# Kernel tuning notes

Measured on AMD Instinct MI355X. Metric: run time of the kernel, lower is better.

The kernel has to match this reference:

```python
import jax, jax.numpy as jnp
import numpy as np

N_NODES = 100000
N_EDGES = 3200000
D_FEAT = 16


def scatter_mean(src, index, num_segments):
    # src: [E, d], index: [E] -> [num_segments, d]; mean over incident edges,
    # with count clamped to 1 (matches torch_scatter.scatter_mean behavior).
    sums = jax.ops.segment_sum(src, index, num_segments=num_segments)
    counts = jax.ops.segment_sum(jnp.ones((src.shape[0],), dtype=src.dtype), index,
                                 num_segments=num_segments)
    return sums / jnp.maximum(counts, 1.0)[:, None]


def setup_inputs() -> dict:
    key = jax.random.key(0)
    k1, k2, k3 = jax.random.split(key, 3)
    predictedTensor = jax.random.normal(k1, (N_NODES, D_FEAT), dtype=jnp.float32)
    inputTensor = jax.random.normal(k2, (N_NODES, D_FEAT), dtype=jnp.float32)
    edge_index = jax.random.randint(k3, (2, N_EDGES), 0, N_NODES, dtype=jnp.int64)
    return {"predictedTensor": predictedTensor, "inputTensor": inputTensor,
            "edge_index": edge_index}


def reference(predictedTensor, inputTensor, edge_index):
    row, col = edge_index[0], edge_index[1]
    n = predictedTensor.shape[0]
    delta_dash = scatter_mean(predictedTensor[row] - predictedTensor[col], row, n)
    delta = scatter_mean(inputTensor[row] - inputTensor[col], row, n)
    diff = delta_dash - delta                      # [N, d]
    return jnp.mean(jnp.sum(diff * diff, axis=1))  # scalar
```

## Files before the change

### kernel.cpp

```cpp
#include <hip/hip_runtime.h>

#define NN 100000
#define CSH 7
#define CNODES 128
#define NC ((NN + CNODES - 1) / CNODES)
#define TPBS 512
#define TPBB 512
#define EPQ 4
#define TILE4 (TPBS * EPQ)
#define TILEE (TILE4 * 4)
#define PADG 16u
#define SEGMAXP 7168
#define SEGMAXP4 (SEGMAXP / 4)
#define ITK 4
#define SENT 0xFFFFFFFFu

__device__ __forceinline__ unsigned f2bf(float f) {
    unsigned u = __float_as_uint(f);
    return (u + 0x7FFFu + ((u >> 16) & 1u)) >> 16;
}
__device__ __forceinline__ unsigned pk(float lo, float hi) {
    return f2bf(lo) | (f2bf(hi) << 16);
}
__device__ __forceinline__ float bflo(unsigned v) { return __uint_as_float(v << 16); }
__device__ __forceinline__ float bfhi(unsigned v) { return __uint_as_float(v & 0xFFFF0000u); }

__global__ void k_init(unsigned* __restrict__ cursor, float* __restrict__ out,
                       uint4* __restrict__ qb) {
    int i = threadIdx.x;
    for (int j = i; j < NC; j += 1024) cursor[j] = 0u;
    if (i == 0) {
        *out = 0.f;
        qb[2 * NN]     = make_uint4(0u, 0u, 0u, 0u);
        qb[2 * NN + 1] = make_uint4(0u, 0u, 0u, 0u);
    }
}

__global__ __launch_bounds__(TPBS) void k_scat1(const float4* __restrict__ pred,
                        const float4* __restrict__ inp, uint4* __restrict__ qb,
                        const int4* __restrict__ row4, const int4* __restrict__ col4,
                        const int* __restrict__ row, const int* __restrict__ col,
                        unsigned* __restrict__ cursor, unsigned* __restrict__ binned,
                        int E, int n8) {
    __shared__ unsigned lcnt[NC], lofs[NC], lpos[NC], gdst[NC];
    __shared__ unsigned stage[TILEE];
    __shared__ unsigned wtot[8], wofs[8];
    int tid = threadIdx.x;
    int lane = tid & 63, wid = tid >> 6;
    int E4 = E >> 2;
    long long base4 = (long long)blockIdx.x * TILE4;
    bool lastblk = (blockIdx.x == gridDim.x - 1);

    for (int i = blockIdx.x * TPBS + tid; i < n8; i += gridDim.x * TPBS) {
        float4 a0 = pred[2 * i], a1 = pred[2 * i + 1];
        float4 b0 = inp[2 * i],  b1 = inp[2 * i + 1];
        uint4 o;
        o.x = pk(a0.x - b0.x, a0.y - b0.y);
        o.y = pk(a0.z - b0.z, a0.w - b0.w);
        o.z = pk(a1.x - b1.x, a1.y - b1.y);
        o.w = pk(a1.z - b1.z, a1.w - b1.w);
        qb[i] = o;
    }

    for (int i = tid; i < NC; i += TPBS) { lcnt[i] = 0u; lpos[i] = 0u; }
    __syncthreads();
    int4 r[EPQ], c[EPQ];
    bool val[EPQ];
    #pragma unroll
    for (int j = 0; j < EPQ; ++j) {
        long long i4 = base4 + (long long)j * TPBS + tid;
        val[j] = (i4 < E4);
        if (val[j]) {
            r[j] = row4[i4]; c[j] = col4[i4];
            atomicAdd(&lcnt[((unsigned)r[j].x) >> CSH], 1u);
            atomicAdd(&lcnt[((unsigned)r[j].y) >> CSH], 1u);
            atomicAdd(&lcnt[((unsigned)r[j].z) >> CSH], 1u);
            atomicAdd(&lcnt[((unsigned)r[j].w) >> CSH], 1u);
        }
    }
    int rt = 0, ct_ = 0;
    bool tval = lastblk && tid < (E & 3);
    if (tval) {
        int e = (E & ~3) + tid;
        rt = row[e]; ct_ = col[e];
        atomicAdd(&lcnt[((unsigned)rt) >> CSH], 1u);
    }
    __syncthreads();
    unsigned v0 = (2 * tid     < NC) ? lcnt[2 * tid]     : 0u;
    unsigned v1 = (2 * tid + 1 < NC) ? lcnt[2 * tid + 1] : 0u;
    unsigned s = v0 + v1;
    unsigned x = s;
    #pragma unroll
    for (int off = 1; off < 64; off <<= 1) {
        unsigned t = __shfl_up(x, off);
        if (lane >= off) x += t;
    }
    if (lane == 63) wtot[wid] = x;
    __syncthreads();
    if (tid < 8) {
        unsigned wv = wtot[tid], wx = wv;
        #pragma unroll
        for (int off = 1; off < 8; off <<= 1) {
            unsigned t = __shfl_up(wx, off);
            if (tid >= off) wx += t;
        }
        wofs[tid] = wx - wv;
    }
    __syncthreads();
    unsigned ex = x - s + wofs[wid];
    if (2 * tid < NC) {
        lofs[2 * tid] = ex;
        unsigned rp = (v0 + PADG - 1u) & ~(PADG - 1u);
        gdst[2 * tid] = rp ? atomicAdd(&cursor[2 * tid], rp) : 0u;
    }
    if (2 * tid + 1 < NC) {
        lofs[2 * tid + 1] = ex + v0;
        unsigned rp = (v1 + PADG - 1u) & ~(PADG - 1u);
        gdst[2 * tid + 1] = rp ? atomicAdd(&cursor[2 * tid + 1], rp) : 0u;
    }
    __syncthreads();
    #pragma unroll
    for (int j = 0; j < EPQ; ++j) {
        if (val[j]) {
            int rr[4] = {r[j].x, r[j].y, r[j].z, r[j].w};
            int cc4[4] = {c[j].x, c[j].y, c[j].z, c[j].w};
            #pragma unroll
            for (int k = 0; k < 4; ++k) {
                unsigned ru = (unsigned)rr[k];
                unsigned b = ru >> CSH;
                unsigned pos = lofs[b] + atomicAdd(&lpos[b], 1u);
                stage[pos] = ((ru & (CNODES - 1u)) << 17) | (unsigned)cc4[k];
            }
        }
    }
    if (tval) {
        unsigned ru = (unsigned)rt;
        unsigned b = ru >> CSH;
        unsigned pos = lofs[b] + atomicAdd(&lpos[b], 1u);
        stage[pos] = ((ru & (CNODES - 1u)) << 17) | (unsigned)ct_;
    }
    __syncthreads();
    for (int i = tid; i < NC; i += TPBS) {
        unsigned cc = lcnt[i];
        unsigned rp = (cc + PADG - 1u) & ~(PADG - 1u);
        unsigned ls = lofs[i];
        unsigned gd = gdst[i];
        if (gd + rp > SEGMAXP) rp = (gd < SEGMAXP) ? (SEGMAXP - gd) : 0u;
        uint4* dst = (uint4*)(binned + (size_t)i * SEGMAXP + gd);
        for (unsigned j = 0; j < rp; j += 4u) {
            uint4 v;
            v.x = (j + 0 < cc) ? stage[ls + j + 0] : SENT;
            v.y = (j + 1 < cc) ? stage[ls + j + 1] : SENT;
            v.z = (j + 2 < cc) ? stage[ls + j + 2] : SENT;
            v.w = (j + 3 < cc) ? stage[ls + j + 3] : SENT;
            dst[j >> 2] = v;
        }
    }
}

__global__ __launch_bounds__(TPBB) void k_bucket(const uint2* __restrict__ qb2,
                         const uint4* __restrict__ binned4,
                         const unsigned* __restrict__ cursor,
                         float* __restrict__ out, int N) {
    __shared__ unsigned ncnt8[8][CNODES];
    __shared__ unsigned ncnt[CNODES], nstart[CNODES];
    __shared__ unsigned scol[SEGMAXP];
    __shared__ float wred[8];
    int tid = threadIdx.x, b = blockIdx.x;
    int lane = tid & 63, wid = tid >> 6;
    for (int i = tid; i < 8 * CNODES; i += TPBB) ((unsigned*)ncnt8)[i] = 0u;
    __syncthreads();
    const uint4* seg4 = binned4 + (size_t)b * SEGMAXP4;
    unsigned m = cursor[b];
    if (m > SEGMAXP) m = SEGMAXP;
    unsigned m4 = m >> 2;
    uint4 it[ITK];
    bool hv[ITK];
    #pragma unroll
    for (int k = 0; k < ITK; ++k) {
        unsigned idx = (unsigned)tid + (unsigned)k * TPBB;
        hv[k] = (idx < m4);
        if (hv[k]) {
            it[k] = seg4[idx];
            if (it[k].x != SENT) atomicAdd(&ncnt8[wid][it[k].x >> 17], 1u);
            if (it[k].y != SENT) atomicAdd(&ncnt8[wid][it[k].y >> 17], 1u);
            if (it[k].z != SENT) atomicAdd(&ncnt8[wid][it[k].z >> 17], 1u);
            if (it[k].w != SENT) atomicAdd(&ncnt8[wid][it[k].w >> 17], 1u);
        }
    }
    __syncthreads();
    if (tid < CNODES) {
        unsigned t0 = 0u;
        #pragma unroll
        for (int w = 0; w < 8; ++w) {
            unsigned c = ncnt8[w][tid];
            ncnt8[w][tid] = t0;
            t0 += c;
        }
        ncnt[tid] = t0;
    }
    __syncthreads();
    if (tid < 64) {
        unsigned c0 = (ncnt[tid * 2] + 3u) & ~3u;
        unsigned c1 = (ncnt[tid * 2 + 1] + 3u) & ~3u;
        unsigned s = c0 + c1;
        unsigned x = s;
        #pragma unroll
        for (int off = 1; off < 64; off <<= 1) {
            unsigned t = __shfl_up(x, off);
            if (tid >= off) x += t;
        }
        unsigned ex = x - s;
        nstart[tid * 2] = ex;
        nstart[tid * 2 + 1] = ex + c0;
    }
    __syncthreads();
    if (tid < CNODES) {
        unsigned ns = nstart[tid];
        #pragma unroll
        for (int w = 0; w < 8; ++w) ncnt8[w][tid] += ns;
    }
    __syncthreads();
    #pragma unroll
    for (int k = 0; k < ITK; ++k) {
        if (hv[k]) {
            if (it[k].x != SENT) { unsigned rk = atomicAdd(&ncnt8[wid][it[k].x >> 17], 1u); scol[rk] = it[k].x & 0x1FFFFu; }
            if (it[k].y != SENT) { unsigned rk = atomicAdd(&ncnt8[wid][it[k].y >> 17], 1u); scol[rk] = it[k].y & 0x1FFFFu; }
            if (it[k].z != SENT) { unsigned rk = atomicAdd(&ncnt8[wid][it[k].z >> 17], 1u); scol[rk] = it[k].z & 0x1FFFFu; }
            if (it[k].w != SENT) { unsigned rk = atomicAdd(&ncnt8[wid][it[k].w >> 17], 1u); scol[rk] = it[k].w & 0x1FFFFu; }
        }
    }
    if (tid < CNODES) {
        unsigned c = ncnt[tid], cp = (c + 3u) & ~3u, st = nstart[tid];
        for (unsigned j = c; j < cp; ++j) scol[st + j] = (unsigned)NN;
    }
    __syncthreads();

    int nl = tid >> 2;
    int p  = tid & 3;
    int n = (b << CSH) + nl;
    unsigned cnt = ncnt[nl], st = nstart[nl];
    float a0 = 0.f, a1 = 0.f, a2 = 0.f, a3 = 0.f;
    for (unsigned i = 0; i < cnt; i += 4u) {
        uint4 cc = *(const uint4*)(scol + st + i);
        uint2 vA = qb2[(size_t)cc.x * 4 + p];
        uint2 vB = qb2[(size_t)cc.y * 4 + p];
        uint2 vC = qb2[(size_t)cc.z * 4 + p];
        uint2 vD = qb2[(size_t)cc.w * 4 + p];
        a0 += bflo(vA.x); a1 += bfhi(vA.x); a2 += bflo(vA.y); a3 += bfhi(vA.y);
        a0 += bflo(vB.x); a1 += bfhi(vB.x); a2 += bflo(vB.y); a3 += bfhi(vB.y);
        a0 += bflo(vC.x); a1 += bfhi(vC.x); a2 += bflo(vC.y); a3 += bfhi(vC.y);
        a0 += bflo(vD.x); a1 += bfhi(vD.x); a2 += bflo(vD.y); a3 += bfhi(vD.y);
    }
    float ss = 0.f;
    if (n < N) {
        uint2 v = qb2[(size_t)n * 4 + p];
        float cf = (float)cnt;
        float d0 = cf * bflo(v.x) - a0, d1 = cf * bfhi(v.x) - a1;
        float d2 = cf * bflo(v.y) - a2, d3 = cf * bfhi(v.y) - a3;
        ss = d0 * d0 + d1 * d1 + d2 * d2 + d3 * d3;
    }
    ss += __shfl_xor(ss, 1);
    ss += __shfl_xor(ss, 2);
    float bss = 0.f;
    if (p == 0 && n < N) {
        float c1f = (cnt > 1u) ? (float)cnt : 1.f;
        bss = ss / (c1f * c1f);
    }
    #pragma unroll
    for (int mm = 4; mm < 64; mm <<= 1) bss += __shfl_xor(bss, mm);
    if (lane == 0) wred[wid] = bss;
    __syncthreads();
    if (tid == 0) {
        float acc = 0.f;
        #pragma unroll
        for (int w = 0; w < 8; ++w) acc += wred[w];
        atomicAdd(out, acc * (1.0f / (float)NN));
    }
}

extern "C" void kernel_launch(void* const* d_in, const int* in_sizes, int n_in,
                              void* d_out, int out_size, void* d_ws, size_t ws_size,
                              hipStream_t stream) {
    const float* pred = (const float*)d_in[0];
    const float* inp  = (const float*)d_in[1];
    const int*   eidx = (const int*)d_in[2];

    const int N = NN;
    const int E = in_sizes[2] / 2;
    const int* row = eidx;
    const int* col = eidx + E;

    size_t off = 0;
    auto alloc = [&](size_t bytes) { void* p = (char*)d_ws + off; off = (off + bytes + 511) & ~(size_t)511; return p; };
    uint4*    qb     = (uint4*)alloc((size_t)(N + 1) * 32);
    unsigned* cursor = (unsigned*)alloc(NC * sizeof(unsigned));
    unsigned* binned = (unsigned*)alloc((size_t)NC * SEGMAXP * sizeof(unsigned));

    k_init<<<1, 1024, 0, stream>>>(cursor, (float*)d_out, qb);

    int n8 = N * 16 / 8;
    int E4 = E >> 2;
    int nsc = (E4 + TILE4 - 1) / TILE4;
    k_scat1<<<nsc, TPBS, 0, stream>>>((const float4*)pred, (const float4*)inp, qb,
                                      (const int4*)row, (const int4*)col, row, col,
                                      cursor, binned, E, n8);

    k_bucket<<<NC, TPBB, 0, stream>>>((const uint2*)qb, (const uint4*)binned, cursor,
                                      (float*)d_out, N);
}
```

Before: 67.72 us.

## Reuse histogram atomic return values as ranks and drop init kernel

```diff
diff --git a/kernel.cpp b/kernel.cpp
--- a/kernel.cpp
+++ b/kernel.cpp
@@ -25,24 +25,13 @@
 __device__ __forceinline__ float bflo(unsigned v) { return __uint_as_float(v << 16); }
 __device__ __forceinline__ float bfhi(unsigned v) { return __uint_as_float(v & 0xFFFF0000u); }
 
-__global__ void k_init(unsigned* __restrict__ cursor, float* __restrict__ out,
-                       uint4* __restrict__ qb) {
-    int i = threadIdx.x;
-    for (int j = i; j < NC; j += 1024) cursor[j] = 0u;
-    if (i == 0) {
-        *out = 0.f;
-        qb[2 * NN]     = make_uint4(0u, 0u, 0u, 0u);
-        qb[2 * NN + 1] = make_uint4(0u, 0u, 0u, 0u);
-    }
-}
-
 __global__ __launch_bounds__(TPBS) void k_scat1(const float4* __restrict__ pred,
                         const float4* __restrict__ inp, uint4* __restrict__ qb,
                         const int4* __restrict__ row4, const int4* __restrict__ col4,
                         const int* __restrict__ row, const int* __restrict__ col,
                         unsigned* __restrict__ cursor, unsigned* __restrict__ binned,
-                        int E, int n8) {
-    __shared__ unsigned lcnt[NC], lofs[NC], lpos[NC], gdst[NC];
+                        float* __restrict__ out, int E, int n8) {
+    __shared__ unsigned lcnt[NC], lofs[NC], gdst[NC];
     __shared__ unsigned stage[TILEE];
     __shared__ unsigned wtot[8], wofs[8];
     int tid = threadIdx.x;
@@ -50,6 +39,12 @@
     int E4 = E >> 2;
     long long base4 = (long long)blockIdx.x * TILE4;
     bool lastblk = (blockIdx.x == gridDim.x - 1);
+
+    if (blockIdx.x == 0 && tid == 0) {
+        *out = 0.f;
+        qb[2 * NN]     = make_uint4(0u, 0u, 0u, 0u);
+        qb[2 * NN + 1] = make_uint4(0u, 0u, 0u, 0u);
+    }
 
     for (int i = blockIdx.x * TPBS + tid; i < n8; i += gridDim.x * TPBS) {
         float4 a0 = pred[2 * i], a1 = pred[2 * i + 1];
@@ -62,9 +57,10 @@
         qb[i] = o;
     }
 
-    for (int i = tid; i < NC; i += TPBS) { lcnt[i] = 0u; lpos[i] = 0u; }
+    for (int i = tid; i < NC; i += TPBS) lcnt[i] = 0u;
     __syncthreads();
     int4 r[EPQ], c[EPQ];
+    uint2 rnk[EPQ];
     bool val[EPQ];
     #pragma unroll
     for (int j = 0; j < EPQ; ++j) {
@@ -72,18 +68,21 @@
         val[j] = (i4 < E4);
         if (val[j]) {
             r[j] = row4[i4]; c[j] = col4[i4];
-            atomicAdd(&lcnt[((unsigned)r[j].x) >> CSH], 1u);
-            atomicAdd(&lcnt[((unsigned)r[j].y) >> CSH], 1u);
-            atomicAdd(&lcnt[((unsigned)r[j].z) >> CSH], 1u);
-            atomicAdd(&lcnt[((unsigned)r[j].w) >> CSH], 1u);
+            unsigned k0 = atomicAdd(&lcnt[((unsigned)r[j].x) >> CSH], 1u);
+            unsigned k1 = atomicAdd(&lcnt[((unsigned)r[j].y) >> CSH], 1u);
+            unsigned k2 = atomicAdd(&lcnt[((unsigned)r[j].z) >> CSH], 1u);
+            unsigned k3 = atomicAdd(&lcnt[((unsigned)r[j].w) >> CSH], 1u);
+            rnk[j].x = k0 | (k1 << 16);
+            rnk[j].y = k2 | (k3 << 16);
         }
     }
     int rt = 0, ct_ = 0;
+    unsigned rnkt = 0u;
     bool tval = lastblk && tid < (E & 3);
     if (tval) {
         int e = (E & ~3) + tid;
         rt = row[e]; ct_ = col[e];
-        atomicAdd(&lcnt[((unsigned)rt) >> CSH], 1u);
+        rnkt = atomicAdd(&lcnt[((unsigned)rt) >> CSH], 1u);
     }
     __syncthreads();
     unsigned v0 = (2 * tid     < NC) ? lcnt[2 * tid]     : 0u;
@@ -122,22 +121,20 @@
     #pragma unroll
     for (int j = 0; j < EPQ; ++j) {
         if (val[j]) {
-            int rr[4] = {r[j].x, r[j].y, r[j].z, r[j].w};
-            int cc4[4] = {c[j].x, c[j].y, c[j].z, c[j].w};
-            #pragma unroll
-            for (int k = 0; k < 4; ++k) {
-                unsigned ru = (unsigned)rr[k];
-                unsigned b = ru >> CSH;
-                unsigned pos = lofs[b] + atomicAdd(&lpos[b], 1u);
-                stage[pos] = ((ru & (CNODES - 1u)) << 17) | (unsigned)cc4[k];
-            }
+            unsigned ru, bb;
+            ru = (unsigned)r[j].x; bb = ru >> CSH;
+            stage[lofs[bb] + (rnk[j].x & 0xFFFFu)] = ((ru & (CNODES - 1u)) << 17) | (unsigned)c[j].x;
+            ru = (unsigned)r[j].y; bb = ru >> CSH;
+            stage[lofs[bb] + (rnk[j].x >> 16)]     = ((ru & (CNODES - 1u)) << 17) | (unsigned)c[j].y;
+            ru = (unsigned)r[j].z; bb = ru >> CSH;
+            stage[lofs[bb] + (rnk[j].y & 0xFFFFu)] = ((ru & (CNODES - 1u)) << 17) | (unsigned)c[j].z;
+            ru = (unsigned)r[j].w; bb = ru >> CSH;
+            stage[lofs[bb] + (rnk[j].y >> 16)]     = ((ru & (CNODES - 1u)) << 17) | (unsigned)c[j].w;
         }
     }
     if (tval) {
-        unsigned ru = (unsigned)rt;
-        unsigned b = ru >> CSH;
-        unsigned pos = lofs[b] + atomicAdd(&lpos[b], 1u);
-        stage[pos] = ((ru & (CNODES - 1u)) << 17) | (unsigned)ct_;
+        unsigned ru = (unsigned)rt, bb = ru >> CSH;
+        stage[lofs[bb] + rnkt] = ((ru & (CNODES - 1u)) << 17) | (unsigned)ct_;
     }
     __syncthreads();
     for (int i = tid; i < NC; i += TPBS) {
@@ -174,60 +171,56 @@
     unsigned m = cursor[b];
     if (m > SEGMAXP) m = SEGMAXP;
     unsigned m4 = m >> 2;
-    uint4 it[ITK];
-    bool hv[ITK];
+    uint2 rk[ITK];
     #pragma unroll
     for (int k = 0; k < ITK; ++k) {
         unsigned idx = (unsigned)tid + (unsigned)k * TPBB;
-        hv[k] = (idx < m4);
-        if (hv[k]) {
-            it[k] = seg4[idx];
-            if (it[k].x != SENT) atomicAdd(&ncnt8[wid][it[k].x >> 17], 1u);
-            if (it[k].y != SENT) atomicAdd(&ncnt8[wid][it[k].y >> 17], 1u);
-            if (it[k].z != SENT) atomicAdd(&ncnt8[wid][it[k].z >> 17], 1u);
-            if (it[k].w != SENT) atomicAdd(&ncnt8[wid][it[k].w >> 17], 1u);
-        }
-    }
-    __syncthreads();
-    if (tid < CNODES) {
-        unsigned t0 = 0u;
+        if (idx < m4) {
+            uint4 v = seg4[idx];
+            unsigned r0 = (v.x != SENT) ? atomicAdd(&ncnt8[wid][v.x >> 17], 1u) : 0u;
+            unsigned r1 = (v.y != SENT) ? atomicAdd(&ncnt8[wid][v.y >> 17], 1u) : 0u;
+            unsigned r2 = (v.z != SENT) ? atomicAdd(&ncnt8[wid][v.z >> 17], 1u) : 0u;
+            unsigned r3 = (v.w != SENT) ? atomicAdd(&ncnt8[wid][v.w >> 17], 1u) : 0u;
+            rk[k].x = r0 | (r1 << 16);
+            rk[k].y = r2 | (r3 << 16);
+        }
+    }
+    __syncthreads();
+    if (tid < 64) {
+        int n0 = 2 * tid, n1 = 2 * tid + 1;
+        unsigned p0[8], p1[8], t0 = 0u, t1 = 0u;
         #pragma unroll
         for (int w = 0; w < 8; ++w) {
-            unsigned c = ncnt8[w][tid];
-            ncnt8[w][tid] = t0;
-            t0 += c;
-        }
-        ncnt[tid] = t0;
-    }
-    __syncthreads();
-    if (tid < 64) {
-        unsigned c0 = (ncnt[tid * 2] + 3u) & ~3u;
-        unsigned c1 = (ncnt[tid * 2 + 1] + 3u) & ~3u;
-        unsigned s = c0 + c1;
-        unsigned x = s;
+            p0[w] = ncnt8[w][n0]; t0 += p0[w];
+            p1[w] = ncnt8[w][n1]; t1 += p1[w];
+        }
+        ncnt[n0] = t0; ncnt[n1] = t1;
+        unsigned c0a = (t0 + 3u) & ~3u, c1a = (t1 + 3u) & ~3u;
+        unsigned s = c0a + c1a, x = s;
         #pragma unroll
         for (int off = 1; off < 64; off <<= 1) {
             unsigned t = __shfl_up(x, off);
             if (tid >= off) x += t;
         }
         unsigned ex = x - s;
-        nstart[tid * 2] = ex;
-        nstart[tid * 2 + 1] = ex + c0;
-    }
-    __syncthreads();
-    if (tid < CNODES) {
-        unsigned ns = nstart[tid];
-        #pragma unroll
-        for (int w = 0; w < 8; ++w) ncnt8[w][tid] += ns;
+        nstart[n0] = ex; nstart[n1] = ex + c0a;
+        unsigned acc = ex;
+        #pragma unroll
+        for (int w = 0; w < 8; ++w) { unsigned cc = p0[w]; ncnt8[w][n0] = acc; acc += cc; }
+        acc = ex + c0a;
+        #pragma unroll
+        for (int w = 0; w < 8; ++w) { unsigned cc = p1[w]; ncnt8[w][n1] = acc; acc += cc; }
     }
     __syncthreads();
     #pragma unroll
     for (int k = 0; k < ITK; ++k) {
-        if (hv[k]) {
-            if (it[k].x != SENT) { unsigned rk = atomicAdd(&ncnt8[wid][it[k].x >> 17], 1u); scol[rk] = it[k].x & 0x1FFFFu; }
-            if (it[k].y != SENT) { unsigned rk = atomicAdd(&ncnt8[wid][it[k].y >> 17], 1u); scol[rk] = it[k].y & 0x1FFFFu; }
-            if (it[k].z != SENT) { unsigned rk = atomicAdd(&ncnt8[wid][it[k].z >> 17], 1u); scol[rk] = it[k].z & 0x1FFFFu; }
-            if (it[k].w != SENT) { unsigned rk = atomicAdd(&ncnt8[wid][it[k].w >> 17], 1u); scol[rk] = it[k].w & 0x1FFFFu; }
+        unsigned idx = (unsigned)tid + (unsigned)k * TPBB;
+        if (idx < m4) {
+            uint4 v = seg4[idx];
+            if (v.x != SENT) scol[ncnt8[wid][v.x >> 17] + (rk[k].x & 0xFFFFu)] = v.x & 0x1FFFFu;
+            if (v.y != SENT) scol[ncnt8[wid][v.y >> 17] + (rk[k].x >> 16)]     = v.y & 0x1FFFFu;
+            if (v.z != SENT) scol[ncnt8[wid][v.z >> 17] + (rk[k].y & 0xFFFFu)] = v.z & 0x1FFFFu;
+            if (v.w != SENT) scol[ncnt8[wid][v.w >> 17] + (rk[k].y >> 16)]     = v.w & 0x1FFFFu;
         }
     }
     if (tid < CNODES) {
@@ -240,13 +233,14 @@
     int p  = tid & 3;
     int n = (b << CSH) + nl;
     unsigned cnt = ncnt[nl], st = nstart[nl];
+    const uint2* qp = qb2 + p;
     float a0 = 0.f, a1 = 0.f, a2 = 0.f, a3 = 0.f;
     for (unsigned i = 0; i < cnt; i += 4u) {
         uint4 cc = *(const uint4*)(scol + st + i);
-        uint2 vA = qb2[(size_t)cc.x * 4 + p];
-        uint2 vB = qb2[(size_t)cc.y * 4 + p];
-        uint2 vC = qb2[(size_t)cc.z * 4 + p];
-        uint2 vD = qb2[(size_t)cc.w * 4 + p];
+        uint2 vA = qp[(size_t)cc.x * 4];
+        uint2 vB = qp[(size_t)cc.y * 4];
+        uint2 vC = qp[(size_t)cc.z * 4];
+        uint2 vD = qp[(size_t)cc.w * 4];
         a0 += bflo(vA.x); a1 += bfhi(vA.x); a2 += bflo(vA.y); a3 += bfhi(vA.y);
         a0 += bflo(vB.x); a1 += bfhi(vB.x); a2 += bflo(vB.y); a3 += bfhi(vB.y);
         a0 += bflo(vC.x); a1 += bfhi(vC.x); a2 += bflo(vC.y); a3 += bfhi(vC.y);
@@ -254,7 +248,7 @@
     }
     float ss = 0.f;
     if (n < N) {
-        uint2 v = qb2[(size_t)n * 4 + p];
+        uint2 v = qp[(size_t)n * 4];
         float cf = (float)cnt;
         float d0 = cf * bflo(v.x) - a0, d1 = cf * bfhi(v.x) - a1;
         float d2 = cf * bflo(v.y) - a2, d3 = cf * bfhi(v.y) - a3;
@@ -297,14 +291,14 @@
     unsigned* cursor = (unsigned*)alloc(NC * sizeof(unsigned));
     unsigned* binned = (unsigned*)alloc((size_t)NC * SEGMAXP * sizeof(unsigned));
 
-    k_init<<<1, 1024, 0, stream>>>(cursor, (float*)d_out, qb);
+    hipMemsetAsync(cursor, 0, NC * sizeof(unsigned), stream);
 
     int n8 = N * 16 / 8;
     int E4 = E >> 2;
     int nsc = (E4 + TILE4 - 1) / TILE4;
     k_scat1<<<nsc, TPBS, 0, stream>>>((const float4*)pred, (const float4*)inp, qb,
                                       (const int4*)row, (const int4*)col, row, col,
-                                      cursor, binned, E, n8);
+                                      cursor, binned, (float*)d_out, E, n8);
 
     k_bucket<<<NC, TPBB, 0, stream>>>((const uint2*)qb, (const uint4*)binned, cursor,
                                       (float*)d_out, N);
```

New measurement: 69.87 us. 1.03x slower.

## Fuse scatter and bucket kernels into one persistent kernel with grid barrier

Applied to the files above, without the earlier changes.

```diff
diff --git a/kernel.cpp b/kernel.cpp
--- a/kernel.cpp
+++ b/kernel.cpp
@@ -5,7 +5,6 @@
 #define CNODES 128
 #define NC ((NN + CNODES - 1) / CNODES)
 #define TPBS 512
-#define TPBB 512
 #define EPQ 4
 #define TILE4 (TPBS * EPQ)
 #define TILEE (TILE4 * 4)
@@ -25,257 +24,270 @@
 __device__ __forceinline__ float bflo(unsigned v) { return __uint_as_float(v << 16); }
 __device__ __forceinline__ float bfhi(unsigned v) { return __uint_as_float(v & 0xFFFF0000u); }
 
-__global__ void k_init(unsigned* __restrict__ cursor, float* __restrict__ out,
-                       uint4* __restrict__ qb) {
-    int i = threadIdx.x;
-    for (int j = i; j < NC; j += 1024) cursor[j] = 0u;
-    if (i == 0) {
-        *out = 0.f;
-        qb[2 * NN]     = make_uint4(0u, 0u, 0u, 0u);
-        qb[2 * NN + 1] = make_uint4(0u, 0u, 0u, 0u);
-    }
-}
-
-__global__ __launch_bounds__(TPBS) void k_scat1(const float4* __restrict__ pred,
+__global__ __launch_bounds__(TPBS) void k_fused(const float4* __restrict__ pred,
                         const float4* __restrict__ inp, uint4* __restrict__ qb,
                         const int4* __restrict__ row4, const int4* __restrict__ col4,
                         const int* __restrict__ row, const int* __restrict__ col,
                         unsigned* __restrict__ cursor, unsigned* __restrict__ binned,
-                        int E, int n8) {
-    __shared__ unsigned lcnt[NC], lofs[NC], lpos[NC], gdst[NC];
-    __shared__ unsigned stage[TILEE];
+                        unsigned* __restrict__ done, float* __restrict__ out,
+                        int E, int n8, int N) {
+    __shared__ unsigned shA[TILEE];
+    __shared__ unsigned shB[4 * NC];
     __shared__ unsigned wtot[8], wofs[8];
+    __shared__ float wred[8];
     int tid = threadIdx.x;
     int lane = tid & 63, wid = tid >> 6;
-    int E4 = E >> 2;
-    long long base4 = (long long)blockIdx.x * TILE4;
-    bool lastblk = (blockIdx.x == gridDim.x - 1);
-
-    for (int i = blockIdx.x * TPBS + tid; i < n8; i += gridDim.x * TPBS) {
-        float4 a0 = pred[2 * i], a1 = pred[2 * i + 1];
-        float4 b0 = inp[2 * i],  b1 = inp[2 * i + 1];
-        uint4 o;
-        o.x = pk(a0.x - b0.x, a0.y - b0.y);
-        o.y = pk(a0.z - b0.z, a0.w - b0.w);
-        o.z = pk(a1.x - b1.x, a1.y - b1.y);
-        o.w = pk(a1.z - b1.z, a1.w - b1.w);
-        qb[i] = o;
+
+    {
+        unsigned* lcnt = shB;
+        unsigned* lofs = shB + NC;
+        unsigned* lpos = shB + 2 * NC;
+        unsigned* gdst = shB + 3 * NC;
+        unsigned* stage = shA;
+        int E4 = E >> 2;
+        long long base4 = (long long)blockIdx.x * TILE4;
+        bool lastblk = (blockIdx.x == gridDim.x - 1);
+
+        if (blockIdx.x == 0 && tid == 0) {
+            *out = 0.f;
+            qb[2 * NN]     = make_uint4(0u, 0u, 0u, 0u);
+            qb[2 * NN + 1] = make_uint4(0u, 0u, 0u, 0u);
+        }
+        for (int i = blockIdx.x * TPBS + tid; i < n8; i += gridDim.x * TPBS) {
+            float4 a0 = pred[2 * i], a1 = pred[2 * i + 1];
+            float4 b0 = inp[2 * i],  b1 = inp[2 * i + 1];
+            uint4 o;
+            o.x = pk(a0.x - b0.x, a0.y - b0.y);
+            o.y = pk(a0.z - b0.z, a0.w - b0.w);
+            o.z = pk(a1.x - b1.x, a1.y - b1.y);
+            o.w = pk(a1.z - b1.z, a1.w - b1.w);
+            qb[i] = o;
+        }
+        for (int i = tid; i < NC; i += TPBS) { lcnt[i] = 0u; lpos[i] = 0u; }
+        __syncthreads();
+        int4 r[EPQ], c[EPQ];
+        bool val[EPQ];
+        #pragma unroll
+        for (int j = 0; j < EPQ; ++j) {
+            long long i4 = base4 + (long long)j * TPBS + tid;
+            val[j] = (i4 < E4);
+            if (val[j]) {
+                r[j] = row4[i4]; c[j] = col4[i4];
+                atomicAdd(&lcnt[((unsigned)r[j].x) >> CSH], 1u);
+                atomicAdd(&lcnt[((unsigned)r[j].y) >> CSH], 1u);
+                atomicAdd(&lcnt[((unsigned)r[j].z) >> CSH], 1u);
+                atomicAdd(&lcnt[((unsigned)r[j].w) >> CSH], 1u);
+            }
+        }
+        int rt = 0, ct_ = 0;
+        bool tval = lastblk && tid < (E & 3);
+        if (tval) {
+            int e = (E & ~3) + tid;
+            rt = row[e]; ct_ = col[e];
+            atomicAdd(&lcnt[((unsigned)rt) >> CSH], 1u);
+        }
+        __syncthreads();
+        unsigned v0 = (2 * tid     < NC) ? lcnt[2 * tid]     : 0u;
+        unsigned v1 = (2 * tid + 1 < NC) ? lcnt[2 * tid + 1] : 0u;
+        unsigned s = v0 + v1;
+        unsigned x = s;
+        #pragma unroll
+        for (int off = 1; off < 64; off <<= 1) {
+            unsigned t = __shfl_up(x, off);
+            if (lane >= off) x += t;
+        }
+        if (lane == 63) wtot[wid] = x;
+        __syncthreads();
+        if (tid < 8) {
+            unsigned wv = wtot[tid], wx = wv;
+            #pragma unroll
+            for (int off = 1; off < 8; off <<= 1) {
+                unsigned t = __shfl_up(wx, off);
+                if (tid >= off) wx += t;
+            }
+            wofs[tid] = wx - wv;
+        }
+        __syncthreads();
+        unsigned ex = x - s + wofs[wid];
+        if (2 * tid < NC) {
+            lofs[2 * tid] = ex;
+            unsigned rp = (v0 + PADG - 1u) & ~(PADG - 1u);
+            gdst[2 * tid] = rp ? atomicAdd(&cursor[2 * tid], rp) : 0u;
+        }
+        if (2 * tid + 1 < NC) {
+            lofs[2 * tid + 1] = ex + v0;
+            unsigned rp = (v1 + PADG - 1u) & ~(PADG - 1u);
+            gdst[2 * tid + 1] = rp ? atomicAdd(&cursor[2 * tid + 1], rp) : 0u;
+        }
+        __syncthreads();
+        #pragma unroll
+        for (int j = 0; j < EPQ; ++j) {
+            if (val[j]) {
+                int rr[4] = {r[j].x, r[j].y, r[j].z, r[j].w};
+                int cc4[4] = {c[j].x, c[j].y, c[j].z, c[j].w};
+                #pragma unroll
+                for (int k = 0; k < 4; ++k) {
+                    unsigned ru = (unsigned)rr[k];
+                    unsigned b = ru >> CSH;
+                    unsigned pos = lofs[b] + atomicAdd(&lpos[b], 1u);
+                    stage[pos] = ((ru & (CNODES - 1u)) << 17) | (unsigned)cc4[k];
+                }
+            }
+        }
+        if (tval) {
+            unsigned ru = (unsigned)rt;
+            unsigned b = ru >> CSH;
+            unsigned pos = lofs[b] + atomicAdd(&lpos[b], 1u);
+            stage[pos] = ((ru & (CNODES - 1u)) << 17) | (unsigned)ct_;
+        }
+        __syncthreads();
+        for (int i = tid; i < NC; i += TPBS) {
+            unsigned cc = lcnt[i];
+            unsigned rp = (cc + PADG - 1u) & ~(PADG - 1u);
+            unsigned ls = lofs[i];
+            unsigned gd = gdst[i];
+            if (gd + rp > SEGMAXP) rp = (gd < SEGMAXP) ? (SEGMAXP - gd) : 0u;
+            uint4* dst = (uint4*)(binned + (size_t)i * SEGMAXP + gd);
+            for (unsigned j = 0; j < rp; j += 4u) {
+                uint4 v;
+                v.x = (j + 0 < cc) ? stage[ls + j + 0] : SENT;
+                v.y = (j + 1 < cc) ? stage[ls + j + 1] : SENT;
+                v.z = (j + 2 < cc) ? stage[ls + j + 2] : SENT;
+                v.w = (j + 3 < cc) ? stage[ls + j + 3] : SENT;
+                dst[j >> 2] = v;
+            }
+        }
+        __syncthreads();
     }
 
-    for (int i = tid; i < NC; i += TPBS) { lcnt[i] = 0u; lpos[i] = 0u; }
-    __syncthreads();
-    int4 r[EPQ], c[EPQ];
-    bool val[EPQ];
-    #pragma unroll
-    for (int j = 0; j < EPQ; ++j) {
-        long long i4 = base4 + (long long)j * TPBS + tid;
-        val[j] = (i4 < E4);
-        if (val[j]) {
-            r[j] = row4[i4]; c[j] = col4[i4];
-            atomicAdd(&lcnt[((unsigned)r[j].x) >> CSH], 1u);
-            atomicAdd(&lcnt[((unsigned)r[j].y) >> CSH], 1u);
-            atomicAdd(&lcnt[((unsigned)r[j].z) >> CSH], 1u);
-            atomicAdd(&lcnt[((unsigned)r[j].w) >> CSH], 1u);
-        }
-    }
-    int rt = 0, ct_ = 0;
-    bool tval = lastblk && tid < (E & 3);
-    if (tval) {
-        int e = (E & ~3) + tid;
-        rt = row[e]; ct_ = col[e];
-        atomicAdd(&lcnt[((unsigned)rt) >> CSH], 1u);
+    if (tid == 0) {
+        __threadfence();
+        atomicAdd(done, 1u);
+        while (atomicAdd(done, 0u) < (unsigned)gridDim.x)
+            __builtin_amdgcn_s_sleep(8);
     }
     __syncthreads();
-    unsigned v0 = (2 * tid     < NC) ? lcnt[2 * tid]     : 0u;
-    unsigned v1 = (2 * tid + 1 < NC) ? lcnt[2 * tid + 1] : 0u;
-    unsigned s = v0 + v1;
-    unsigned x = s;
-    #pragma unroll
-    for (int off = 1; off < 64; off <<= 1) {
-        unsigned t = __shfl_up(x, off);
-        if (lane >= off) x += t;
-    }
-    if (lane == 63) wtot[wid] = x;
+    __threadfence();
     __syncthreads();
-    if (tid < 8) {
-        unsigned wv = wtot[tid], wx = wv;
-        #pragma unroll
-        for (int off = 1; off < 8; off <<= 1) {
-            unsigned t = __shfl_up(wx, off);
-            if (tid >= off) wx += t;
-        }
-        wofs[tid] = wx - wv;
-    }
-    __syncthreads();
-    unsigned ex = x - s + wofs[wid];
-    if (2 * tid < NC) {
-        lofs[2 * tid] = ex;
-        unsigned rp = (v0 + PADG - 1u) & ~(PADG - 1u);
-        gdst[2 * tid] = rp ? atomicAdd(&cursor[2 * tid], rp) : 0u;
-    }
-    if (2 * tid + 1 < NC) {
-        lofs[2 * tid + 1] = ex + v0;
-        unsigned rp = (v1 + PADG - 1u) & ~(PADG - 1u);
-        gdst[2 * tid + 1] = rp ? atomicAdd(&cursor[2 * tid + 1], rp) : 0u;
-    }
-    __syncthreads();
-    #pragma unroll
-    for (int j = 0; j < EPQ; ++j) {
-        if (val[j]) {
-            int rr[4] = {r[j].x, r[j].y, r[j].z, r[j].w};
-            int cc4[4] = {c[j].x, c[j].y, c[j].z, c[j].w};
-            #pragma unroll
-            for (int k = 0; k < 4; ++k) {
-                unsigned ru = (unsigned)rr[k];
-                unsigned b = ru >> CSH;
-                unsigned pos = lofs[b] + atomicAdd(&lpos[b], 1u);
-                stage[pos] = ((ru & (CNODES - 1u)) << 17) | (unsigned)cc4[k];
-            }
-        }
-    }
-    if (tval) {
-        unsigned ru = (unsigned)rt;
-        unsigned b = ru >> CSH;
-        unsigned pos = lofs[b] + atomicAdd(&lpos[b], 1u);
-        stage[pos] = ((ru & (CNODES - 1u)) << 17) | (unsigned)ct_;
-    }
-    __syncthreads();
-    for (int i = tid; i < NC; i += TPBS) {
-        unsigned cc = lcnt[i];
-        unsigned rp = (cc + PADG - 1u) & ~(PADG - 1u);
-        unsigned ls = lofs[i];
-        unsigned gd = gdst[i];
-        if (gd + rp > SEGMAXP) rp = (gd < SEGMAXP) ? (SEGMAXP - gd) : 0u;
-        uint4* dst = (uint4*)(binned + (size_t)i * SEGMAXP + gd);
-        for (unsigned j = 0; j < rp; j += 4u) {
-            uint4 v;
-            v.x = (j + 0 < cc) ? stage[ls + j + 0] : SENT;
-            v.y = (j + 1 < cc) ? stage[ls + j + 1] : SENT;
-            v.z = (j + 2 < cc) ? stage[ls + j + 2] : SENT;
-            v.w = (j + 3 < cc) ? stage[ls + j + 3] : SENT;
-            dst[j >> 2] = v;
-        }
-    }
-}
-
-__global__ __launch_bounds__(TPBB) void k_bucket(const uint2* __restrict__ qb2,
-                         const uint4* __restrict__ binned4,
-                         const unsigned* __restrict__ cursor,
-                         float* __restrict__ out, int N) {
-    __shared__ unsigned ncnt8[8][CNODES];
-    __shared__ unsigned ncnt[CNODES], nstart[CNODES];
-    __shared__ unsigned scol[SEGMAXP];
-    __shared__ float wred[8];
-    int tid = threadIdx.x, b = blockIdx.x;
-    int lane = tid & 63, wid = tid >> 6;
-    for (int i = tid; i < 8 * CNODES; i += TPBB) ((unsigned*)ncnt8)[i] = 0u;
-    __syncthreads();
-    const uint4* seg4 = binned4 + (size_t)b * SEGMAXP4;
-    unsigned m = cursor[b];
-    if (m > SEGMAXP) m = SEGMAXP;
-    unsigned m4 = m >> 2;
-    uint4 it[ITK];
-    bool hv[ITK];
-    #pragma unroll
-    for (int k = 0; k < ITK; ++k) {
-        unsigned idx = (unsigned)tid + (unsigned)k * TPBB;
-        hv[k] = (idx < m4);
-        if (hv[k]) {
-            it[k] = seg4[idx];
-            if (it[k].x != SENT) atomicAdd(&ncnt8[wid][it[k].x >> 17], 1u);
-            if (it[k].y != SENT) atomicAdd(&ncnt8[wid][it[k].y >> 17], 1u);
-            if (it[k].z != SENT) atomicAdd(&ncnt8[wid][it[k].z >> 17], 1u);
-            if (it[k].w != SENT) atomicAdd(&ncnt8[wid][it[k].w >> 17], 1u);
-        }
-    }
-    __syncthreads();
-    if (tid < CNODES) {
-        unsigned t0 = 0u;
-        #pragma unroll
-        for (int w = 0; w < 8; ++w) {
-            unsigned c = ncnt8[w][tid];
-            ncnt8[w][tid] = t0;
-            t0 += c;
-        }
-        ncnt[tid] = t0;
-    }
-    __syncthreads();
-    if (tid < 64) {
-        unsigned c0 = (ncnt[tid * 2] + 3u) & ~3u;
-        unsigned c1 = (ncnt[tid * 2 + 1] + 3u) & ~3u;
-        unsigned s = c0 + c1;
-        unsigned x = s;
-        #pragma unroll
-        for (int off = 1; off < 64; off <<= 1) {
-            unsigned t = __shfl_up(x, off);
-            if (tid >= off) x += t;
-        }
-        unsigned ex = x - s;
-        nstart[tid * 2] = ex;
-        nstart[tid * 2 + 1] = ex + c0;
-    }
-    __syncthreads();
-    if (tid < CNODES) {
-        unsigned ns = nstart[tid];
-        #pragma unroll
-        for (int w = 0; w < 8; ++w) ncnt8[w][tid] += ns;
-    }
-    __syncthreads();
-    #pragma unroll
-    for (int k = 0; k < ITK; ++k) {
-        if (hv[k]) {
-            if (it[k].x != SENT) { unsigned rk = atomicAdd(&ncnt8[wid][it[k].x >> 17], 1u); scol[rk] = it[k].x & 0x1FFFFu; }
-            if (it[k].y != SENT) { unsigned rk = atomicAdd(&ncnt8[wid][it[k].y >> 17], 1u); scol[rk] = it[k].y & 0x1FFFFu; }
-            if (it[k].z != SENT) { unsigned rk = atomicAdd(&ncnt8[wid][it[k].z >> 17], 1u); scol[rk] = it[k].z & 0x1FFFFu; }
-            if (it[k].w != SENT) { unsigned rk = atomicAdd(&ncnt8[wid][it[k].w >> 17], 1u); scol[rk] = it[k].w & 0x1FFFFu; }
-        }
-    }
-    if (tid < CNODES) {
-        unsigned c = ncnt[tid], cp = (c + 3u) & ~3u, st = nstart[tid];
-        for (unsigned j = c; j < cp; ++j) scol[st + j] = (unsigned)NN;
-    }
-    __syncthreads();
-
-    int nl = tid >> 2;
-    int p  = tid & 3;
-    int n = (b << CSH) + nl;
-    unsigned cnt = ncnt[nl], st = nstart[nl];
-    float a0 = 0.f, a1 = 0.f, a2 = 0.f, a3 = 0.f;
-    for (unsigned i = 0; i < cnt; i += 4u) {
-        uint4 cc = *(const uint4*)(scol + st + i);
-        uint2 vA = qb2[(size_t)cc.x * 4 + p];
-        uint2 vB = qb2[(size_t)cc.y * 4 + p];
-        uint2 vC = qb2[(size_t)cc.z * 4 + p];
-        uint2 vD = qb2[(size_t)cc.w * 4 + p];
-        a0 += bflo(vA.x); a1 += bfhi(vA.x); a2 += bflo(vA.y); a3 += bfhi(vA.y);
-        a0 += bflo(vB.x); a1 += bfhi(vB.x); a2 += bflo(vB.y); a3 += bfhi(vB.y);
-        a0 += bflo(vC.x); a1 += bfhi(vC.x); a2 += bflo(vC.y); a3 += bfhi(vC.y);
-        a0 += bflo(vD.x); a1 += bfhi(vD.x); a2 += bflo(vD.y); a3 += bfhi(vD.y);
-    }
-    float ss = 0.f;
-    if (n < N) {
-        uint2 v = qb2[(size_t)n * 4 + p];
-        float cf = (float)cnt;
-        float d0 = cf * bflo(v.x) - a0, d1 = cf * bfhi(v.x) - a1;
-        float d2 = cf * bflo(v.y) - a2, d3 = cf * bfhi(v.y) - a3;
-        ss = d0 * d0 + d1 * d1 + d2 * d2 + d3 * d3;
-    }
-    ss += __shfl_xor(ss, 1);
-    ss += __shfl_xor(ss, 2);
-    float bss = 0.f;
-    if (p == 0 && n < N) {
-        float c1f = (cnt > 1u) ? (float)cnt : 1.f;
-        bss = ss / (c1f * c1f);
-    }
-    #pragma unroll
-    for (int mm = 4; mm < 64; mm <<= 1) bss += __shfl_xor(bss, mm);
-    if (lane == 0) wred[wid] = bss;
-    __syncthreads();
-    if (tid == 0) {
-        float acc = 0.f;
-        #pragma unroll
-        for (int w = 0; w < 8; ++w) acc += wred[w];
-        atomicAdd(out, acc * (1.0f / (float)NN));
+
+    unsigned (*ncnt8)[CNODES] = (unsigned (*)[CNODES])shB;
+    unsigned* ncnt   = shB + 8 * CNODES;
+    unsigned* nstart = shB + 8 * CNODES + CNODES;
+    unsigned* scol   = shA;
+    const uint2* qb2 = (const uint2*)qb;
+
+    for (int b = blockIdx.x; b < NC; b += gridDim.x) {
+        __syncthreads();
+        for (int i = tid; i < 8 * CNODES; i += TPBS) ((unsigned*)ncnt8)[i] = 0u;
+        __syncthreads();
+        const uint4* seg4 = (const uint4*)(binned) + (size_t)b * SEGMAXP4;
+        unsigned m = cursor[b];
+        if (m > SEGMAXP) m = SEGMAXP;
+        unsigned m4 = m >> 2;
+        uint4 it[ITK];
+        bool hv[ITK];
+        #pragma unroll
+        for (int k = 0; k < ITK; ++k) {
+            unsigned idx = (unsigned)tid + (unsigned)k * TPBS;
+            hv[k] = (idx < m4);
+            if (hv[k]) {
+                it[k] = seg4[idx];
+                if (it[k].x != SENT) atomicAdd(&ncnt8[wid][it[k].x >> 17], 1u);
+                if (it[k].y != SENT) atomicAdd(&ncnt8[wid][it[k].y >> 17], 1u);
+                if (it[k].z != SENT) atomicAdd(&ncnt8[wid][it[k].z >> 17], 1u);
+                if (it[k].w != SENT) atomicAdd(&ncnt8[wid][it[k].w >> 17], 1u);
+            }
+        }
+        __syncthreads();
+        if (tid < CNODES) {
+            unsigned t0 = 0u;
+            #pragma unroll
+            for (int w = 0; w < 8; ++w) {
+                unsigned c = ncnt8[w][tid];
+                ncnt8[w][tid] = t0;
+                t0 += c;
+            }
+            ncnt[tid] = t0;
+        }
+        __syncthreads();
+        if (tid < 64) {
+            unsigned c0 = (ncnt[tid * 2] + 3u) & ~3u;
+            unsigned c1 = (ncnt[tid * 2 + 1] + 3u) & ~3u;
+            unsigned s = c0 + c1;
+            unsigned x = s;
+            #pragma unroll
+            for (int off = 1; off < 64; off <<= 1) {
+                unsigned t = __shfl_up(x, off);
+                if (tid >= off) x += t;
+            }
+            unsigned ex = x - s;
+            nstart[tid * 2] = ex;
+            nstart[tid * 2 + 1] = ex + c0;
+        }
+        __syncthreads();
+        if (tid < CNODES) {
+            unsigned ns = nstart[tid];
+            #pragma unroll
+            for (int w = 0; w < 8; ++w) ncnt8[w][tid] += ns;
+        }
+        __syncthreads();
+        #pragma unroll
+        for (int k = 0; k < ITK; ++k) {
+            if (hv[k]) {
+                if (it[k].x != SENT) { unsigned rk = atomicAdd(&ncnt8[wid][it[k].x >> 17], 1u); scol[rk] = it[k].x & 0x1FFFFu; }
+                if (it[k].y != SENT) { unsigned rk = atomicAdd(&ncnt8[wid][it[k].y >> 17], 1u); scol[rk] = it[k].y & 0x1FFFFu; }
+                if (it[k].z != SENT) { unsigned rk = atomicAdd(&ncnt8[wid][it[k].z >> 17], 1u); scol[rk] = it[k].z & 0x1FFFFu; }
+                if (it[k].w != SENT) { unsigned rk = atomicAdd(&ncnt8[wid][it[k].w >> 17], 1u); scol[rk] = it[k].w & 0x1FFFFu; }
+            }
+        }
+        if (tid < CNODES) {
+            unsigned c = ncnt[tid], cp = (c + 3u) & ~3u, st = nstart[tid];
+            for (unsigned j = c; j < cp; ++j) scol[st + j] = (unsigned)NN;
+        }
+        __syncthreads();
+
+        int nl = tid >> 2;
+        int p  = tid & 3;
+        int n = (b << CSH) + nl;
+        unsigned cnt = ncnt[nl], st = nstart[nl];
+        const uint2* qp = qb2 + p;
+        float a0 = 0.f, a1 = 0.f, a2 = 0.f, a3 = 0.f;
+        for (unsigned i = 0; i < cnt; i += 4u) {
+            uint4 cc = *(const uint4*)(scol + st + i);
+            uint2 vA = qp[(size_t)cc.x * 4];
+            uint2 vB = qp[(size_t)cc.y * 4];
+            uint2 vC = qp[(size_t)cc.z * 4];
+            uint2 vD = qp[(size_t)cc.w * 4];
+            a0 += bflo(vA.x); a1 += bfhi(vA.x); a2 += bflo(vA.y); a3 += bfhi(vA.y);
+            a0 += bflo(vB.x); a1 += bfhi(vB.x); a2 += bflo(vB.y); a3 += bfhi(vB.y);
+            a0 += bflo(vC.x); a1 += bfhi(vC.x); a2 += bflo(vC.y); a3 += bfhi(vC.y);
+            a0 += bflo(vD.x); a1 += bfhi(vD.x); a2 += bflo(vD.y); a3 += bfhi(vD.y);
+        }
+        float ss = 0.f;
+        if (n < N) {
+            uint2 v = qp[(size_t)n * 4];
+            float cf = (float)cnt;
+            float d0 = cf * bflo(v.x) - a0, d1 = cf * bfhi(v.x) - a1;
+            float d2 = cf * bflo(v.y) - a2, d3 = cf * bfhi(v.y) - a3;
+            ss = d0 * d0 + d1 * d1 + d2 * d2 + d3 * d3;
+        }
+        ss += __shfl_xor(ss, 1);
+        ss += __shfl_xor(ss, 2);
+        float bss = 0.f;
+        if (p == 0 && n < N) {
+            float c1f = (cnt > 1u) ? (float)cnt : 1.f;
+            bss = ss / (c1f * c1f);
+        }
+        #pragma unroll
+        for (int mm = 4; mm < 64; mm <<= 1) bss += __shfl_xor(bss, mm);
+        if (lane == 0) wred[wid] = bss;
+        __syncthreads();
+        if (tid == 0) {
+            float acc = 0.f;
+            #pragma unroll
+            for (int w = 0; w < 8; ++w) acc += wred[w];
+            atomicAdd(out, acc * (1.0f / (float)NN));
+        }
     }
 }
 
@@ -294,18 +306,16 @@
     size_t off = 0;
     auto alloc = [&](size_t bytes) { void* p = (char*)d_ws + off; off = (off + bytes + 511) & ~(size_t)511; return p; };
     uint4*    qb     = (uint4*)alloc((size_t)(N + 1) * 32);
-    unsigned* cursor = (unsigned*)alloc(NC * sizeof(unsigned));
+    unsigned* cursor = (unsigned*)alloc((NC + 16) * sizeof(unsigned));
     unsigned* binned = (unsigned*)alloc((size_t)NC * SEGMAXP * sizeof(unsigned));
-
-    k_init<<<1, 1024, 0, stream>>>(cursor, (float*)d_out, qb);
+    unsigned* done   = cursor + NC;
+
+    hipMemsetAsync(cursor, 0, (NC + 16) * sizeof(unsigned), stream);
 
     int n8 = N * 16 / 8;
     int E4 = E >> 2;
     int nsc = (E4 + TILE4 - 1) / TILE4;
-    k_scat1<<<nsc, TPBS, 0, stream>>>((const float4*)pred, (const float4*)inp, qb,
+    k_fused<<<nsc, TPBS, 0, stream>>>((const float4*)pred, (const float4*)inp, qb,
                                       (const int4*)row, (const int4*)col, row, col,
-                                      cursor, binned, E, n8);
-
-    k_bucket<<<NC, TPBB, 0, stream>>>((const uint2*)qb, (const uint4*)binned, cursor,
-                                      (float*)d_out, N);
+                                      cursor, binned, done, (float*)d_out, E, n8, N);
 }
```

New measurement: 157.9 us. 2.33x slower.
